# Kernel tuning notes

Measured on AMD Instinct MI355X. Metric: run time of the kernel, lower is better.

Reference implementation:

```python
import jax, jax.numpy as jnp
import numpy as np

N_NODES = 50000
N_EDGES = 600000
N_GRAPHS = 512
D_IN = 128
D_H = 128
D_OUT = 10
N_LAYERS = 3
BN_EPS = 1e-5


def setup_inputs() -> dict:
    key = jax.random.key(0)
    ks = jax.random.split(key, 16)
    x = jax.random.normal(ks[0], (N_NODES, D_IN), dtype=jnp.float32)
    edge_index = jax.random.randint(ks[1], (2, N_EDGES), 0, N_NODES)
    # deterministic sorted batch assignment -> every graph non-empty
    batch = (jnp.arange(N_NODES) * N_GRAPHS) // N_NODES
    s = 1.0 / np.sqrt(D_H)
    w_in = jax.random.normal(ks[2], (D_IN, D_H), dtype=jnp.float32) * s
    b_in = jnp.zeros((D_H,), jnp.float32)
    conv_w = jax.random.normal(ks[3], (N_LAYERS, D_H, D_H), dtype=jnp.float32) * s
    conv_b = jnp.zeros((N_LAYERS, D_H), jnp.float32)
    bn_g = jnp.ones((N_LAYERS, D_H), jnp.float32)
    bn_b = jnp.zeros((N_LAYERS, D_H), jnp.float32)
    fc1_w = jax.random.normal(ks[4], (2 * D_H, D_H), dtype=jnp.float32) * (1.0 / np.sqrt(2 * D_H))
    fc1_b = jnp.zeros((D_H,), jnp.float32)
    fc2_w = jax.random.normal(ks[5], (D_H, D_OUT), dtype=jnp.float32) * s
    fc2_b = jnp.zeros((D_OUT,), jnp.float32)
    return {"x": x, "edge_index": edge_index, "batch": batch, "n_graphs": N_GRAPHS,
            "w_in": w_in, "b_in": b_in, "conv_w": conv_w, "conv_b": conv_b,
            "bn_g": bn_g, "bn_b": bn_b, "fc1_w": fc1_w, "fc1_b": fc1_b,
            "fc2_w": fc2_w, "fc2_b": fc2_b}


def reference(x, edge_index, batch, n_graphs, w_in, b_in, conv_w, conv_b,
              bn_g, bn_b, fc1_w, fc1_b, fc2_w, fc2_b):
    n = x.shape[0]
    loop = jnp.arange(n)
    src = jnp.concatenate([edge_index[0], loop])  # self-loops as in PyG GCNConv
    dst = jnp.concatenate([edge_index[1], loop])
    deg = jax.ops.segment_sum(jnp.ones_like(dst, x.dtype), dst, num_segments=n)
    dinv = jax.lax.rsqrt(deg)  # deg >= 1 due to self-loops
    enorm = dinv[src] * dinv[dst]  # (E+N,)

    h = jax.nn.relu(x @ w_in + b_in)
    for i in range(N_LAYERS):
        res = h
        m = h @ conv_w[i]
        # gather -> scale -> scatter-add (symmetric-normalized GCN propagation)
        m = jax.ops.segment_sum(m[src] * enorm[:, None], dst, num_segments=n) + conv_b[i]
        # batchnorm (training-mode batch statistics)
        mu = jnp.mean(m, axis=0)
        var = jnp.mean(jnp.square(m - mu), axis=0)
        m = (m - mu) * jax.lax.rsqrt(var + BN_EPS) * bn_g[i] + bn_b[i]
        m = jax.nn.relu(m)  # dropout is identity in eval
        h = m + res if i > 0 else m

    cnt = jax.ops.segment_sum(jnp.ones((n,), h.dtype), batch, num_segments=n_graphs)
    g_mean = jax.ops.segment_sum(h, batch, num_segments=n_graphs) / cnt[:, None]
    g_max = jax.ops.segment_max(h, batch, num_segments=n_graphs)
    g = jnp.concatenate([g_mean, g_max], axis=1)  # (G, 2*D_H)
    g = jax.nn.relu(g @ fc1_w + fc1_b)
    return g @ fc2_w + fc2_b
```

## Files before the change

### kernel.cpp

```cpp
#include <hip/hip_runtime.h>
#include <hip/hip_bf16.h>
#include <hip/hip_fp16.h>

#define N_NODES 50000
#define N_EDGES 600000
#define N_GRAPHS 512
#define DH 128
#define SLOTS 64
#define NCOPY 8
#define FILL_BLOCKS ((N_EDGES + 255) / 256)
#define WCVT_BLOCKS ((4 * DH * DH) / 256)
#define PROP_BLOCKS (N_NODES / 16)

typedef __attribute__((ext_vector_type(8))) short bf16x8;
typedef __attribute__((ext_vector_type(4))) float fx4;
typedef __attribute__((ext_vector_type(8))) _Float16 hx8;

__device__ __forceinline__ short f2b(float f) {
    union { __hip_bfloat16 b; short s; } u;
    u.b = __float2bfloat16(f);
    return u.s;
}

__device__ __forceinline__ void bn_coef(const float* __restrict__ sums,
                                        const float* __restrict__ gamma,
                                        const float* __restrict__ beta,
                                        int c, float& sA, float& sB) {
    float s = 0.f, q = 0.f;
#pragma unroll
    for (int k = 0; k < NCOPY; ++k) { s += sums[k * 256 + c]; q += sums[k * 256 + DH + c]; }
    const float invn = 1.f / (float)N_NODES;
    float mean = s * invn;
    float var = q * invn - mean * mean;
    sA = gamma[c] * rsqrtf(var + 1e-5f);
    sB = beta[c] - mean * sA;
}

__global__ void k_build(const int* __restrict__ src, const int* __restrict__ dst,
                        int* __restrict__ fill, int* __restrict__ csr,
                        const float* __restrict__ w_in, const float* __restrict__ conv_w,
                        __hip_bfloat16* __restrict__ Wp) {
    int b = blockIdx.x;
    if (b < FILL_BLOCKS) {
        int e = b * 256 + threadIdx.x;
        if (e < N_EDGES) {
            int v = dst[e];
            int pos = atomicAdd(&fill[v], 1);
            if (pos < SLOTS) csr[v * SLOTS + pos] = src[e];
        }
    } else {
        int id = (b - FILL_BLOCKS) * 256 + threadIdx.x;
        int mat = id >> 14, rem = id & 16383;
        int n = rem >> 7, k = rem & 127;
        const float* s = (mat == 0) ? w_in : (conv_w + (mat - 1) * DH * DH);
        Wp[id] = __float2bfloat16(s[k * DH + n]);
    }
}

template <int MODE>
__global__ __launch_bounds__(256) void k_gemm(const void* __restrict__ Av,
                                              const __hip_bfloat16* __restrict__ Wp,
                                              const float* __restrict__ bias,
                                              const float* __restrict__ sums,
                                              const float* __restrict__ gamma,
                                              const float* __restrict__ beta,
                                              _Float16* __restrict__ Hout,
                                              _Float16* __restrict__ Cm) {
    __shared__ __align__(16) float sAl[DH], sBl[DH];
    if (MODE >= 2) {
        if (threadIdx.x < DH) {
            float sA, sB;
            bn_coef(sums, gamma, beta, threadIdx.x, sA, sB);
            sAl[threadIdx.x] = sA;
            sBl[threadIdx.x] = sB;
        }
        __syncthreads();
    }
    int wave = blockIdx.x * 4 + (threadIdx.x >> 6);
    if (wave >= N_NODES / 16) return;
    int lane = threadIdx.x & 63;
    int r = lane & 15, gq = lane >> 4;
    const int row0 = wave * 16;

    const short* wp = (const short*)Wp;
    bf16x8 Bf[8][4];
#pragma unroll
    for (int t = 0; t < 8; ++t)
#pragma unroll
        for (int q = 0; q < 4; ++q)
            Bf[t][q] = *(const bf16x8*)(wp + (t * 16 + r) * DH + q * 32 + gq * 8);

    fx4 acc[8];
#pragma unroll
    for (int t = 0; t < 8; ++t) acc[t] = (fx4){0.f, 0.f, 0.f, 0.f};

#pragma unroll
    for (int q = 0; q < 4; ++q) {
        const int cb = q * 32 + gq * 8;
        float a[8];
        if (MODE == 0) {
            const float* arow = (const float*)Av + (size_t)(row0 + r) * DH + cb;
            fx4 a0 = *(const fx4*)(arow);
            fx4 a1 = *(const fx4*)(arow + 4);
#pragma unroll
            for (int j = 0; j < 4; ++j) { a[j] = a0[j]; a[4 + j] = a1[j]; }
        } else {
            const _Float16* arow = (const _Float16*)Av + (size_t)(row0 + r) * DH + cb;
            hx8 av = *(const hx8*)(arow);
#pragma unroll
            for (int j = 0; j < 8; ++j) a[j] = (float)av[j];
        }
        if (MODE >= 2) {
            fx4 sA0 = *(const fx4*)(sAl + cb);
            fx4 sA1 = *(const fx4*)(sAl + cb + 4);
            fx4 sB0 = *(const fx4*)(sBl + cb);
            fx4 sB1 = *(const fx4*)(sBl + cb + 4);
#pragma unroll
            for (int j = 0; j < 4; ++j) {
                a[j]     = fmaxf(a[j] * sA0[j] + sB0[j], 0.f);
                a[4 + j] = fmaxf(a[4 + j] * sA1[j] + sB1[j], 0.f);
            }
            _Float16* hrow = Hout + (size_t)(row0 + r) * DH + cb;
            if (MODE == 3) {
                hx8 rv = *(const hx8*)hrow;
#pragma unroll
                for (int j = 0; j < 8; ++j) a[j] += (float)rv[j];
            }
            hx8 hv;
#pragma unroll
            for (int j = 0; j < 8; ++j) hv[j] = (_Float16)a[j];
            *(hx8*)hrow = hv;
        }
        bf16x8 af;
#pragma unroll
        for (int j = 0; j < 8; ++j) af[j] = f2b(a[j]);
#pragma unroll
        for (int t = 0; t < 8; ++t)
            acc[t] = __builtin_amdgcn_mfma_f32_16x16x32_bf16(af, Bf[t][q], acc[t], 0, 0, 0);
    }
#pragma unroll
    for (int t = 0; t < 8; ++t) {
#pragma unroll
        for (int rr = 0; rr < 4; ++rr) {
            int orow = row0 + 4 * gq + rr;
            int ocol = t * 16 + r;
            float v = acc[t][rr];
            if (MODE == 0) v = fmaxf(v + bias[ocol], 0.f);
            Cm[(size_t)orow * DH + ocol] = (_Float16)v;
        }
    }
}

__global__ __launch_bounds__(256) void k_prop(const _Float16* __restrict__ m,
                                              const int* __restrict__ csr,
                                              const int* __restrict__ deg,
                                              _Float16* __restrict__ agg,
                                              float* __restrict__ sums) {
    int g = threadIdx.x >> 4;
    int lane = threadIdx.x & 15;
    int v = blockIdx.x * 16 + g;
    int dvi = deg[v];
    float dv = rsqrtf((float)(dvi + 1));
    hx8 self = ((const hx8*)(m + (size_t)v * DH))[lane];
    float acc[8];
#pragma unroll
    for (int j = 0; j < 8; ++j) acc[j] = dv * (float)self[j];
    int d = dvi > SLOTS ? SLOTS : dvi;
    const int* nb = csr + (size_t)v * SLOTS;
    int i = 0;
    for (; i + 3 < d; i += 4) {
        int4 uu = *(const int4*)(nb + i);
        float e0 = rsqrtf((float)(deg[uu.x] + 1));
        float e1 = rsqrtf((float)(deg[uu.y] + 1));
        float e2 = rsqrtf((float)(deg[uu.z] + 1));
        float e3 = rsqrtf((float)(deg[uu.w] + 1));
        hx8 r0 = ((const hx8*)(m + (size_t)uu.x * DH))[lane];
        hx8 r1 = ((const hx8*)(m + (size_t)uu.y * DH))[lane];
        hx8 r2 = ((const hx8*)(m + (size_t)uu.z * DH))[lane];
        hx8 r3 = ((const hx8*)(m + (size_t)uu.w * DH))[lane];
#pragma unroll
        for (int j = 0; j < 8; ++j)
            acc[j] += e0 * (float)r0[j] + e1 * (float)r1[j] + e2 * (float)r2[j] + e3 * (float)r3[j];
    }
    for (; i < d; ++i) {
        int u = nb[i];
        float eu = rsqrtf((float)(deg[u] + 1));
        hx8 ru = ((const hx8*)(m + (size_t)u * DH))[lane];
#pragma unroll
        for (int j = 0; j < 8; ++j) acc[j] += eu * (float)ru[j];
    }
    float s[8], q2[8];
    hx8 ov;
#pragma unroll
    for (int j = 0; j < 8; ++j) {
        float o = dv * acc[j];
        ov[j] = (_Float16)o;
        s[j] = o;
        q2[j] = o * o;
    }
    ((hx8*)(agg + (size_t)v * DH))[lane] = ov;

#pragma unroll
    for (int j = 0; j < 8; ++j) {
        s[j] += __shfl_xor(s[j], 16);
        s[j] += __shfl_xor(s[j], 32);
        q2[j] += __shfl_xor(q2[j], 16);
        q2[j] += __shfl_xor(q2[j], 32);
    }
    __shared__ float lsum[4][DH], lsq[4][DH];
    int wv = threadIdx.x >> 6, wl = threadIdx.x & 63;
    if (wl < 16) {
#pragma unroll
        for (int j = 0; j < 8; ++j) {
            lsum[wv][wl * 8 + j] = s[j];
            lsq[wv][wl * 8 + j] = q2[j];
        }
    }
    __syncthreads();
    if (threadIdx.x < DH) {
        int c = threadIdx.x;
        float ts = lsum[0][c] + lsum[1][c] + lsum[2][c] + lsum[3][c];
        float tq = lsq[0][c] + lsq[1][c] + lsq[2][c] + lsq[3][c];
        float* dstp = sums + (blockIdx.x & (NCOPY - 1)) * 256;
        atomicAdd(&dstp[c], ts);
        atomicAdd(&dstp[DH + c], tq);
    }
}

__global__ __launch_bounds__(256) void k_poolhead(const _Float16* __restrict__ agg,
                                                  const float* __restrict__ sums,
                                                  const float* __restrict__ gamma,
                                                  const float* __restrict__ beta,
                                                  const _Float16* __restrict__ hres,
                                                  const float* __restrict__ fc1w,
                                                  const float* __restrict__ fc1b,
                                                  const float* __restrict__ fc2w,
                                                  const float* __restrict__ fc2b,
                                                  float* __restrict__ out) {
    __shared__ __align__(16) float sAl[DH], sBl[DH];
    if (threadIdx.x < DH) {
        float sA, sB;
        bn_coef(sums, gamma, beta, threadIdx.x, sA, sB);
        sAl[threadIdx.x] = sA;
        sBl[threadIdx.x] = sB;
    }
    __syncthreads();

    int gr = blockIdx.x;
    int start = (gr * N_NODES + N_GRAPHS - 1) / N_GRAPHS;
    int end = ((gr + 1) * N_NODES + N_GRAPHS - 1) / N_GRAPHS;
    int grp = threadIdx.x >> 4, lane = threadIdx.x & 15;
    float sA[8], sB[8];
#pragma unroll
    for (int j = 0; j < 8; ++j) { sA[j] = sAl[lane * 8 + j]; sB[j] = sBl[lane * 8 + j]; }
    float sm[8], mx[8];
#pragma unroll
    for (int j = 0; j < 8; ++j) { sm[j] = 0.f; mx[j] = -3.4e38f; }
    for (int v = start + grp; v < end; v += 16) {
        hx8 a = ((const hx8*)(agg + (size_t)v * DH))[lane];
        hx8 r = ((const hx8*)(hres + (size_t)v * DH))[lane];
#pragma unroll
        for (int j = 0; j < 8; ++j) {
            float hv = fmaxf((float)a[j] * sA[j] + sB[j], 0.f) + (float)r[j];
            sm[j] += hv;
            mx[j] = fmaxf(mx[j], hv);
        }
    }
#pragma unroll
    for (int j = 0; j < 8; ++j) {
        sm[j] += __shfl_xor(sm[j], 16);
        sm[j] += __shfl_xor(sm[j], 32);
        mx[j] = fmaxf(mx[j], __shfl_xor(mx[j], 16));
        mx[j] = fmaxf(mx[j], __shfl_xor(mx[j], 32));
    }
    __shared__ float psum[4][DH], pmax[4][DH];
    __shared__ float gl[2 * DH], tt[DH];
    int wv = threadIdx.x >> 6, wl = threadIdx.x & 63;
    if (wl < 16) {
#pragma unroll
        for (int j = 0; j < 8; ++j) {
            psum[wv][wl * 8 + j] = sm[j];
            pmax[wv][wl * 8 + j] = mx[j];
        }
    }
    __syncthreads();
    if (threadIdx.x < DH) {
        int c = threadIdx.x;
        float ts = psum[0][c] + psum[1][c] + psum[2][c] + psum[3][c];
        float tm = fmaxf(fmaxf(pmax[0][c], pmax[1][c]), fmaxf(pmax[2][c], pmax[3][c]));
        gl[c] = ts / (float)(end - start);
        gl[DH + c] = tm;
    }
    __syncthreads();
    if (threadIdx.x < DH) {
        int j = threadIdx.x;
        float acc = fc1b[j];
        for (int k = 0; k < 2 * DH; ++k) acc += gl[k] * fc1w[k * DH + j];
        tt[j] = fmaxf(acc, 0.f);
    }
    __syncthreads();
    if (threadIdx.x < 10) {
        int j = threadIdx.x;
        float o = fc2b[j];
        for (int k = 0; k < DH; ++k) o += tt[k] * fc2w[k * 10 + j];
        out[gr * 10 + j] = o;
    }
}

extern "C" void kernel_launch(void* const* d_in, const int* in_sizes, int n_in,
                              void* d_out, int out_size, void* d_ws, size_t ws_size,
                              hipStream_t stream) {
    const float* x      = (const float*)d_in[0];
    const int*   ei     = (const int*)d_in[1];
    const float* w_in   = (const float*)d_in[4];
    const float* b_in   = (const float*)d_in[5];
    const float* conv_w = (const float*)d_in[6];
    const float* bn_g   = (const float*)d_in[8];
    const float* bn_b   = (const float*)d_in[9];
    const float* fc1w   = (const float*)d_in[10];
    const float* fc1b   = (const float*)d_in[11];
    const float* fc2w   = (const float*)d_in[12];
    const float* fc2b   = (const float*)d_in[13];
    float* out = (float*)d_out;

    const int* e_src = ei;
    const int* e_dst = ei + N_EDGES;

    char* ws = (char*)d_ws;
    size_t o = 0;
    auto alloc = [&](size_t bytes) { size_t r = o; o += (bytes + 255) & ~(size_t)255; return r; };
    size_t o_fill   = alloc(N_NODES * 4);
    size_t o_bnsum  = alloc(3 * NCOPY * 256 * 4);
    size_t zero_end = o;
    size_t o_csr    = alloc((size_t)N_NODES * SLOTS * 4);
    size_t o_wp     = alloc(4 * DH * DH * 2);
    size_t o_h      = alloc((size_t)N_NODES * DH * 2);
    size_t o_m      = alloc((size_t)N_NODES * DH * 2);
    size_t o_agg    = alloc((size_t)N_NODES * DH * 2);
    (void)ws_size;

    int*   fill   = (int*)(ws + o_fill);
    float* bnsum  = (float*)(ws + o_bnsum);
    int*   csr    = (int*)(ws + o_csr);
    __hip_bfloat16* wp = (__hip_bfloat16*)(ws + o_wp);
    _Float16* h   = (_Float16*)(ws + o_h);
    _Float16* m   = (_Float16*)(ws + o_m);
    _Float16* agg = (_Float16*)(ws + o_agg);

    hipMemsetAsync(ws, 0, zero_end, stream);

    k_build<<<FILL_BLOCKS + WCVT_BLOCKS, 256, 0, stream>>>(e_src, e_dst, fill, csr,
                                                           w_in, conv_w, wp);

    const int gemm_blocks = (N_NODES / 16 + 3) / 4;

    k_gemm<0><<<gemm_blocks, 256, 0, stream>>>(x, wp, b_in, nullptr, nullptr, nullptr,
                                               nullptr, h);

    k_gemm<1><<<gemm_blocks, 256, 0, stream>>>(h, wp + 1 * DH * DH, nullptr, nullptr, nullptr,
                                               nullptr, nullptr, m);
    k_prop<<<PROP_BLOCKS, 256, 0, stream>>>(m, csr, fill, agg, bnsum);

    k_gemm<2><<<gemm_blocks, 256, 0, stream>>>(agg, wp + 2 * DH * DH, nullptr, bnsum,
                                               bn_g, bn_b, h, m);
    k_prop<<<PROP_BLOCKS, 256, 0, stream>>>(m, csr, fill, agg, bnsum + NCOPY * 256);

    k_gemm<3><<<gemm_blocks, 256, 0, stream>>>(agg, wp + 3 * DH * DH, nullptr, bnsum + NCOPY * 256,
                                               bn_g + DH, bn_b + DH, h, m);
    k_prop<<<PROP_BLOCKS, 256, 0, stream>>>(m, csr, fill, agg, bnsum + 2 * NCOPY * 256);

    k_poolhead<<<N_GRAPHS, 256, 0, stream>>>(agg, bnsum + 2 * NCOPY * 256,
                                             bn_g + 2 * DH, bn_b + 2 * DH, h,
                                             fc1w, fc1b, fc2w, fc2b, out);
}
```

Before: 313.8 us.

## Fuse input and first conv GEMMs via LDS, prescale messages by source dinv

The input projection and the first conv GEMM now run in one kernel. The intermediate 16-row tile is staged in a swizzled LDS buffer, so the h activation never makes a round trip through global memory. Each GEMM epilogue also multiplies the output rows by rsqrt(deg+1) of the source node. This lets the propagation kernel drop its per-edge degree gathers and rsqrt calls. The cost is a block-wide sync and a second weight-fragment load in the fused kernel.

```diff
diff --git a/kernel.cpp b/kernel.cpp
--- a/kernel.cpp
+++ b/kernel.cpp
@@ -11,6 +11,7 @@
 #define FILL_BLOCKS ((N_EDGES + 255) / 256)
 #define WCVT_BLOCKS ((4 * DH * DH) / 256)
 #define PROP_BLOCKS (N_NODES / 16)
+#define N_WAVES (N_NODES / 16)
 
 typedef __attribute__((ext_vector_type(8))) short bf16x8;
 typedef __attribute__((ext_vector_type(4))) float fx4;
@@ -57,96 +58,172 @@
     }
 }
 
-template <int MODE>
-__global__ __launch_bounds__(256) void k_gemm(const void* __restrict__ Av,
-                                              const __hip_bfloat16* __restrict__ Wp,
-                                              const float* __restrict__ bias,
-                                              const float* __restrict__ sums,
-                                              const float* __restrict__ gamma,
-                                              const float* __restrict__ beta,
-                                              _Float16* __restrict__ Hout,
-                                              _Float16* __restrict__ Cm) {
-    __shared__ __align__(16) float sAl[DH], sBl[DH];
-    if (MODE >= 2) {
-        if (threadIdx.x < DH) {
-            float sA, sB;
-            bn_coef(sums, gamma, beta, threadIdx.x, sA, sB);
-            sAl[threadIdx.x] = sA;
-            sBl[threadIdx.x] = sB;
-        }
-        __syncthreads();
-    }
-    int wave = blockIdx.x * 4 + (threadIdx.x >> 6);
-    if (wave >= N_NODES / 16) return;
+__global__ __launch_bounds__(256) void k_gemm01(const float* __restrict__ x,
+                                                const __hip_bfloat16* __restrict__ Wp0,
+                                                const float* __restrict__ bias,
+                                                const __hip_bfloat16* __restrict__ Wp1,
+                                                const int* __restrict__ deg,
+                                                _Float16* __restrict__ Cm) {
+    __shared__ _Float16 hlds[4][16 * DH];
+    int w = threadIdx.x >> 6;
+    int wave = blockIdx.x * 4 + w;
+    if (wave > N_WAVES - 1) wave = N_WAVES - 1;
     int lane = threadIdx.x & 63;
     int r = lane & 15, gq = lane >> 4;
     const int row0 = wave * 16;
 
-    const short* wp = (const short*)Wp;
+    const short* wp0 = (const short*)Wp0;
     bf16x8 Bf[8][4];
 #pragma unroll
     for (int t = 0; t < 8; ++t)
 #pragma unroll
         for (int q = 0; q < 4; ++q)
-            Bf[t][q] = *(const bf16x8*)(wp + (t * 16 + r) * DH + q * 32 + gq * 8);
+            Bf[t][q] = *(const bf16x8*)(wp0 + (t * 16 + r) * DH + q * 32 + gq * 8);
 
     fx4 acc[8];
 #pragma unroll
     for (int t = 0; t < 8; ++t) acc[t] = (fx4){0.f, 0.f, 0.f, 0.f};
 
+    const float* arow = x + (size_t)(row0 + r) * DH;
 #pragma unroll
     for (int q = 0; q < 4; ++q) {
         const int cb = q * 32 + gq * 8;
-        float a[8];
-        if (MODE == 0) {
-            const float* arow = (const float*)Av + (size_t)(row0 + r) * DH + cb;
-            fx4 a0 = *(const fx4*)(arow);
-            fx4 a1 = *(const fx4*)(arow + 4);
-#pragma unroll
-            for (int j = 0; j < 4; ++j) { a[j] = a0[j]; a[4 + j] = a1[j]; }
-        } else {
-            const _Float16* arow = (const _Float16*)Av + (size_t)(row0 + r) * DH + cb;
-            hx8 av = *(const hx8*)(arow);
-#pragma unroll
-            for (int j = 0; j < 8; ++j) a[j] = (float)av[j];
-        }
-        if (MODE >= 2) {
-            fx4 sA0 = *(const fx4*)(sAl + cb);
-            fx4 sA1 = *(const fx4*)(sAl + cb + 4);
-            fx4 sB0 = *(const fx4*)(sBl + cb);
-            fx4 sB1 = *(const fx4*)(sBl + cb + 4);
-#pragma unroll
-            for (int j = 0; j < 4; ++j) {
-                a[j]     = fmaxf(a[j] * sA0[j] + sB0[j], 0.f);
-                a[4 + j] = fmaxf(a[4 + j] * sA1[j] + sB1[j], 0.f);
-            }
-            _Float16* hrow = Hout + (size_t)(row0 + r) * DH + cb;
-            if (MODE == 3) {
-                hx8 rv = *(const hx8*)hrow;
-#pragma unroll
-                for (int j = 0; j < 8; ++j) a[j] += (float)rv[j];
-            }
-            hx8 hv;
-#pragma unroll
-            for (int j = 0; j < 8; ++j) hv[j] = (_Float16)a[j];
-            *(hx8*)hrow = hv;
-        }
+        fx4 a0 = *(const fx4*)(arow + cb);
+        fx4 a1 = *(const fx4*)(arow + cb + 4);
         bf16x8 af;
-#pragma unroll
-        for (int j = 0; j < 8; ++j) af[j] = f2b(a[j]);
+        af[0] = f2b(a0[0]); af[1] = f2b(a0[1]); af[2] = f2b(a0[2]); af[3] = f2b(a0[3]);
+        af[4] = f2b(a1[0]); af[5] = f2b(a1[1]); af[6] = f2b(a1[2]); af[7] = f2b(a1[3]);
 #pragma unroll
         for (int t = 0; t < 8; ++t)
             acc[t] = __builtin_amdgcn_mfma_f32_16x16x32_bf16(af, Bf[t][q], acc[t], 0, 0, 0);
     }
+    char* base = (char*)&hlds[w][0];
+#pragma unroll
+    for (int t = 0; t < 8; ++t) {
+#pragma unroll
+        for (int rr = 0; rr < 4; ++rr) {
+            int row = 4 * gq + rr;
+            int col = t * 16 + r;
+            float v = fmaxf(acc[t][rr] + bias[col], 0.f);
+            int off = (row * 256 + col * 2) ^ ((row & 15) << 4);
+            *(_Float16*)(base + off) = (_Float16)v;
+        }
+    }
+    const short* wp1 = (const short*)Wp1;
+#pragma unroll
+    for (int t = 0; t < 8; ++t)
+#pragma unroll
+        for (int q = 0; q < 4; ++q)
+            Bf[t][q] = *(const bf16x8*)(wp1 + (t * 16 + r) * DH + q * 32 + gq * 8);
+    __syncthreads();
+#pragma unroll
+    for (int t = 0; t < 8; ++t) acc[t] = (fx4){0.f, 0.f, 0.f, 0.f};
+#pragma unroll
+    for (int q = 0; q < 4; ++q) {
+        int off = (r * 256 + (q * 32 + gq * 8) * 2) ^ ((r & 15) << 4);
+        hx8 av = *(const hx8*)(base + off);
+        bf16x8 af;
+#pragma unroll
+        for (int j = 0; j < 8; ++j) af[j] = f2b((float)av[j]);
+#pragma unroll
+        for (int t = 0; t < 8; ++t)
+            acc[t] = __builtin_amdgcn_mfma_f32_16x16x32_bf16(af, Bf[t][q], acc[t], 0, 0, 0);
+    }
+    float di[4];
+#pragma unroll
+    for (int rr = 0; rr < 4; ++rr)
+        di[rr] = rsqrtf((float)(deg[row0 + 4 * gq + rr] + 1));
 #pragma unroll
     for (int t = 0; t < 8; ++t) {
 #pragma unroll
         for (int rr = 0; rr < 4; ++rr) {
             int orow = row0 + 4 * gq + rr;
             int ocol = t * 16 + r;
-            float v = acc[t][rr];
-            if (MODE == 0) v = fmaxf(v + bias[ocol], 0.f);
-            Cm[(size_t)orow * DH + ocol] = (_Float16)v;
+            Cm[(size_t)orow * DH + ocol] = (_Float16)(acc[t][rr] * di[rr]);
+        }
+    }
+}
+
+template <int RES>
+__global__ __launch_bounds__(256) void k_gemmbn(const _Float16* __restrict__ Av,
+                                                const __hip_bfloat16* __restrict__ Wp,
+                                                const float* __restrict__ sums,
+                                                const float* __restrict__ gamma,
+                                                const float* __restrict__ beta,
+                                                const int* __restrict__ deg,
+                                                _Float16* __restrict__ Hout,
+                                                _Float16* __restrict__ Cm) {
+    __shared__ __align__(16) float sAl[DH], sBl[DH];
+    if (threadIdx.x < DH) {
+        float sA, sB;
+        bn_coef(sums, gamma, beta, threadIdx.x, sA, sB);
+        sAl[threadIdx.x] = sA;
+        sBl[threadIdx.x] = sB;
+    }
+    __syncthreads();
+    int wave = blockIdx.x * 4 + (threadIdx.x >> 6);
+    if (wave >= N_WAVES) return;
+    int lane = threadIdx.x & 63;
+    int r = lane & 15, gq = lane >> 4;
+    const int row0 = wave * 16;
+
+    const short* wp = (const short*)Wp;
+    bf16x8 Bf[8][4];
+#pragma unroll
+    for (int t = 0; t < 8; ++t)
+#pragma unroll
+        for (int q = 0; q < 4; ++q)
+            Bf[t][q] = *(const bf16x8*)(wp + (t * 16 + r) * DH + q * 32 + gq * 8);
+
+    fx4 acc[8];
+#pragma unroll
+    for (int t = 0; t < 8; ++t) acc[t] = (fx4){0.f, 0.f, 0.f, 0.f};
+
+#pragma unroll
+    for (int q = 0; q < 4; ++q) {
+        const int cb = q * 32 + gq * 8;
+        const _Float16* arow = Av + (size_t)(row0 + r) * DH + cb;
+        hx8 av = *(const hx8*)(arow);
+        float a[8];
+#pragma unroll
+        for (int j = 0; j < 8; ++j) a[j] = (float)av[j];
+        fx4 sA0 = *(const fx4*)(sAl + cb);
+        fx4 sA1 = *(const fx4*)(sAl + cb + 4);
+        fx4 sB0 = *(const fx4*)(sBl + cb);
+        fx4 sB1 = *(const fx4*)(sBl + cb + 4);
+#pragma unroll
+        for (int j = 0; j < 4; ++j) {
+            a[j]     = fmaxf(a[j] * sA0[j] + sB0[j], 0.f);
+            a[4 + j] = fmaxf(a[4 + j] * sA1[j] + sB1[j], 0.f);
+        }
+        _Float16* hrow = Hout + (size_t)(row0 + r) * DH + cb;
+        if (RES) {
+            hx8 rv = *(const hx8*)hrow;
+#pragma unroll
+            for (int j = 0; j < 8; ++j) a[j] += (float)rv[j];
+        }
+        hx8 hv;
+#pragma unroll
+        for (int j = 0; j < 8; ++j) hv[j] = (_Float16)a[j];
+        *(hx8*)hrow = hv;
+        bf16x8 af;
+#pragma unroll
+        for (int j = 0; j < 8; ++j) af[j] = f2b(a[j]);
+#pragma unroll
+        for (int t = 0; t < 8; ++t)
+            acc[t] = __builtin_amdgcn_mfma_f32_16x16x32_bf16(af, Bf[t][q], acc[t], 0, 0, 0);
+    }
+    float di[4];
+#pragma unroll
+    for (int rr = 0; rr < 4; ++rr)
+        di[rr] = rsqrtf((float)(deg[row0 + 4 * gq + rr] + 1));
+#pragma unroll
+    for (int t = 0; t < 8; ++t) {
+#pragma unroll
+        for (int rr = 0; rr < 4; ++rr) {
+            int orow = row0 + 4 * gq + rr;
+            int ocol = t * 16 + r;
+            Cm[(size_t)orow * DH + ocol] = (_Float16)(acc[t][rr] * di[rr]);
         }
     }
 }
@@ -164,30 +241,25 @@
     hx8 self = ((const hx8*)(m + (size_t)v * DH))[lane];
     float acc[8];
 #pragma unroll
-    for (int j = 0; j < 8; ++j) acc[j] = dv * (float)self[j];
+    for (int j = 0; j < 8; ++j) acc[j] = (float)self[j];
     int d = dvi > SLOTS ? SLOTS : dvi;
     const int* nb = csr + (size_t)v * SLOTS;
     int i = 0;
     for (; i + 3 < d; i += 4) {
         int4 uu = *(const int4*)(nb + i);
-        float e0 = rsqrtf((float)(deg[uu.x] + 1));
-        float e1 = rsqrtf((float)(deg[uu.y] + 1));
-        float e2 = rsqrtf((float)(deg[uu.z] + 1));
-        float e3 = rsqrtf((float)(deg[uu.w] + 1));
         hx8 r0 = ((const hx8*)(m + (size_t)uu.x * DH))[lane];
         hx8 r1 = ((const hx8*)(m + (size_t)uu.y * DH))[lane];
         hx8 r2 = ((const hx8*)(m + (size_t)uu.z * DH))[lane];
         hx8 r3 = ((const hx8*)(m + (size_t)uu.w * DH))[lane];
 #pragma unroll
         for (int j = 0; j < 8; ++j)
-            acc[j] += e0 * (float)r0[j] + e1 * (float)r1[j] + e2 * (float)r2[j] + e3 * (float)r3[j];
+            acc[j] += (float)r0[j] + (float)r1[j] + (float)r2[j] + (float)r3[j];
     }
     for (; i < d; ++i) {
         int u = nb[i];
-        float eu = rsqrtf((float)(deg[u] + 1));
         hx8 ru = ((const hx8*)(m + (size_t)u * DH))[lane];
 #pragma unroll
-        for (int j = 0; j < 8; ++j) acc[j] += eu * (float)ru[j];
+        for (int j = 0; j < 8; ++j) acc[j] += (float)ru[j];
     }
     float s[8], q2[8];
     hx8 ov;
@@ -352,21 +424,17 @@
     k_build<<<FILL_BLOCKS + WCVT_BLOCKS, 256, 0, stream>>>(e_src, e_dst, fill, csr,
                                                            w_in, conv_w, wp);
 
-    const int gemm_blocks = (N_NODES / 16 + 3) / 4;
-
-    k_gemm<0><<<gemm_blocks, 256, 0, stream>>>(x, wp, b_in, nullptr, nullptr, nullptr,
-                                               nullptr, h);
-
-    k_gemm<1><<<gemm_blocks, 256, 0, stream>>>(h, wp + 1 * DH * DH, nullptr, nullptr, nullptr,
-                                               nullptr, nullptr, m);
+    const int gemm_blocks = (N_WAVES + 3) / 4;
+
+    k_gemm01<<<gemm_blocks, 256, 0, stream>>>(x, wp, b_in, wp + 1 * DH * DH, fill, m);
     k_prop<<<PROP_BLOCKS, 256, 0, stream>>>(m, csr, fill, agg, bnsum);
 
-    k_gemm<2><<<gemm_blocks, 256, 0, stream>>>(agg, wp + 2 * DH * DH, nullptr, bnsum,
-                                               bn_g, bn_b, h, m);
+    k_gemmbn<0><<<gemm_blocks, 256, 0, stream>>>(agg, wp + 2 * DH * DH, bnsum,
+                                                 bn_g, bn_b, fill, h, m);
     k_prop<<<PROP_BLOCKS, 256, 0, stream>>>(m, csr, fill, agg, bnsum + NCOPY * 256);
 
-    k_gemm<3><<<gemm_blocks, 256, 0, stream>>>(agg, wp + 3 * DH * DH, nullptr, bnsum + NCOPY * 256,
-                                               bn_g + DH, bn_b + DH, h, m);
+    k_gemmbn<1><<<gemm_blocks, 256, 0, stream>>>(agg, wp + 3 * DH * DH, bnsum + NCOPY * 256,
+                                                 bn_g + DH, bn_b + DH, fill, h, m);
     k_prop<<<PROP_BLOCKS, 256, 0, stream>>>(m, csr, fill, agg, bnsum + 2 * NCOPY * 256);
 
     k_poolhead<<<N_GRAPHS, 256, 0, stream>>>(agg, bnsum + 2 * NCOPY * 256,
```

New measurement: 313.9 us. No clear change (+0.0%).
